# Performance work log

Hardware: AMD Instinct MI355X
Metric: run time of the kernel (lower is better)

Reference implementation:

```python
import jax, jax.numpy as jnp
import numpy as np

C = 1.0           # Poincare ball curvature magnitude (k = -1/c with c=1)
MIN_NORM = 1e-15
PROJ_EPS = 4e-3   # geoopt float32 boundary eps


def _artanh(x):
    return jnp.arctanh(jnp.clip(x, -1.0 + 1e-7, 1.0 - 1e-7))


def _norm(x):
    return jnp.maximum(jnp.linalg.norm(x, axis=-1, keepdims=True), MIN_NORM)


def mobius_matvec(W, x, c=C):
    # geoopt pmath.mobius_matvec with k=-c
    sc = jnp.sqrt(c)
    x_norm = _norm(x)
    Mx = x @ W.T
    Mx_norm = _norm(Mx)
    return jnp.tanh(Mx_norm / x_norm * _artanh(sc * x_norm)) * Mx / (Mx_norm * sc)


def mobius_add(x, y, c=C):
    x2 = jnp.sum(x * x, axis=-1, keepdims=True)
    y2 = jnp.sum(y * y, axis=-1, keepdims=True)
    xy = jnp.sum(x * y, axis=-1, keepdims=True)
    num = (1.0 + 2.0 * c * xy + c * y2) * x + (1.0 - c * x2) * y
    den = 1.0 + 2.0 * c * xy + c * c * x2 * y2
    return num / jnp.maximum(den, MIN_NORM)


def project(x, c=C):
    norm = _norm(x)
    maxnorm = (1.0 - PROJ_EPS) / jnp.sqrt(c)
    return jnp.where(norm > maxnorm, x / norm * maxnorm, x)


def expmap0(u, c=C):
    sc = jnp.sqrt(c)
    un = _norm(u)
    return jnp.tanh(sc * un) * u / (sc * un)


def mobius_linear(x, W, b, c=C):
    # hyperbolic_input=True, hyperbolic_bias=True, nonlin=None
    out = mobius_matvec(W, x, c)
    out = mobius_add(out, b, c)
    return project(out, c)


def setup_inputs() -> dict:
    key = jax.random.key(0)
    ks = jax.random.split(key, 7)
    N, D = 2048, 1024        # batch*tlen, input_size
    V = 32000                # output_size (vocab)
    SLEN, B, CV = 512, 32, 500
    hidden = jax.random.normal(ks[0], (N, D), jnp.float32) * 0.1
    hidden = project(hidden)
    attn = jax.random.uniform(ks[1], (N, SLEN), jnp.float32)
    src_map = jax.random.uniform(ks[2], (SLEN, B, CV), jnp.float32)
    W = jax.random.normal(ks[3], (V, D), jnp.float32) * 0.01
    b = expmap0(jax.random.normal(ks[4], (V,), jnp.float32) / 4.0)
    Wc = jax.random.normal(ks[5], (1, D), jnp.float32) * 0.01
    bc = expmap0(jax.random.normal(ks[6], (1,), jnp.float32) / 4.0)
    return {"hidden": hidden, "attn": attn, "src_map": src_map,
            "W": W, "b": b, "Wc": Wc, "bc": bc, "pad_idx": 1}


def reference(hidden, attn, src_map, W, b, Wc, bc, pad_idx):
    slen, batch, cvocab = src_map.shape
    logits = mobius_linear(hidden, W, b)                  # (N, V)
    logits = logits.at[:, pad_idx].set(-jnp.inf)
    prob = jax.nn.softmax(logits, axis=1)
    p_copy = jax.nn.sigmoid(mobius_linear(hidden, Wc, bc))  # (N, 1)
    out_prob = prob * (1.0 - p_copy)
    mul_attn = attn * p_copy                              # (N, slen)
    a = mul_attn.reshape(-1, batch, slen)                 # (tlen, batch, slen)
    copy_prob = jnp.einsum('tbs,sbc->tbc', a, src_map).reshape(-1, cvocab)
    return jnp.concatenate([out_prob, copy_prob], axis=1)
```

## Files before the change

kernel.cpp:

```cpp
#include <hip/hip_runtime.h>
#include <stdint.h>

#define N_ROWS   2048
#define D_IN     1024
#define V_OUT    32000
#define SLEN_C   512
#define BATCH_C  32
#define CVOC     500
#define OUT_COLS 32500

#define MIN_NORM_F 1e-15f
#define PROJ_EPS_F 4e-3f

typedef __bf16 bf16x8_t __attribute__((ext_vector_type(8)));
typedef float  f32x4_t  __attribute__((ext_vector_type(4)));
typedef unsigned short ushort8_t __attribute__((ext_vector_type(8)));

__device__ __forceinline__ unsigned short f2bf(float f) {
    uint32_t b = __float_as_uint(f);
    b += 0x7FFFu + ((b >> 16) & 1u);
    return (unsigned short)(b >> 16);
}
__device__ __forceinline__ float bf2f(unsigned short u) {
    return __uint_as_float(((uint32_t)u) << 16);
}
__device__ __forceinline__ float wave_sum(float v) {
#pragma unroll
    for (int off = 32; off > 0; off >>= 1) v += __shfl_down(v, off, 64);
    return v;
}

__device__ __forceinline__ void load_lds16(const void* g, void* l) {
    __builtin_amdgcn_global_load_lds(
        (const __attribute__((address_space(1))) void*)g,
        (__attribute__((address_space(3))) void*)l, 16, 0, 0);
}

__global__ __launch_bounds__(256)
void cast_f32_to_bf16(const float* __restrict__ src, unsigned short* __restrict__ dst, int n4) {
    int i = blockIdx.x * blockDim.x + threadIdx.x;
    int stride = gridDim.x * blockDim.x;
    for (; i < n4; i += stride) {
        float4 v = ((const float4*)src)[i];
        ushort4 o;
        o.x = f2bf(v.x); o.y = f2bf(v.y); o.z = f2bf(v.z); o.w = f2bf(v.w);
        ((ushort4*)dst)[i] = o;
    }
}

__global__ __launch_bounds__(256)
void row_stats(const float* __restrict__ hidden, const float* __restrict__ Wc,
               const float* __restrict__ bc_in, float* __restrict__ g_arr,
               float* __restrict__ pc_arr) {
    __shared__ float red[8];
    const int n = blockIdx.x;
    const int tid = threadIdx.x;
    float4 hv = *(const float4*)(hidden + (size_t)n * D_IN + tid * 4);
    float4 wv = *(const float4*)(Wc + tid * 4);
    float s = hv.x * hv.x + hv.y * hv.y + hv.z * hv.z + hv.w * hv.w;
    float d = hv.x * wv.x + hv.y * wv.y + hv.z * wv.z + hv.w * wv.w;
    s = wave_sum(s); d = wave_sum(d);
    const int w = tid >> 6, l = tid & 63;
    if (l == 0) { red[w] = s; red[4 + w] = d; }
    __syncthreads();
    if (tid == 0) {
        float S  = red[0] + red[1] + red[2] + red[3];
        float Dc = red[4] + red[5] + red[6] + red[7];
        float xn = fmaxf(sqrtf(S), MIN_NORM_F);
        float xc = fminf(xn, 1.f - 1e-7f);
        float at = 0.5f * logf((1.f + xc) / (1.f - xc));
        float g = at / xn;
        float mxn = fmaxf(fabsf(Dc), MIN_NORM_F);
        float res = tanhf(mxn * g) * (Dc / mxn);
        float bcv = bc_in[0];
        float x2 = res * res, y2 = bcv * bcv, xyv = res * bcv;
        float num = (1.f + 2.f * xyv + y2) * res + (1.f - x2) * bcv;
        float dn  = fmaxf(1.f + 2.f * xyv + x2 * y2, MIN_NORM_F);
        float o = num / dn;
        float an = fmaxf(fabsf(o), MIN_NORM_F);
        float mxp = 1.f - PROJ_EPS_F;
        if (an > mxp) o = o / an * mxp;
        pc_arr[n] = 1.f / (1.f + expf(-o));
        g_arr[n]  = g;
    }
}


#define STG_A(bufi, chunk, kti) \
    load_lds16(Ag + (size_t)(am0 + ((chunk) << 6) + wave8 + srow) * D_IN + ((kti) << 6) + sk, \
               &Asmem[bufi][(((chunk) << 6) + wave8) << 6])
#define STG_B(bufi, chunk, kti) \
    load_lds16(Bg + (size_t)(bn0 + ((chunk) << 6) + wave8 + srow) * D_IN + ((kti) << 6) + sk, \
               &Bsmem[bufi][(((chunk) << 6) + wave8) << 6])

#define VMCNT(N) \
    __builtin_amdgcn_sched_barrier(0); \
    asm volatile("s_waitcnt vmcnt(" #N ")" ::: "memory"); \
    __builtin_amdgcn_sched_barrier(0);

#define RD_A(RB, MH) \
    _Pragma("unroll") for (int i = 0; i < 4; ++i) { \
        const int r_ = (wm + (MH)*64 + i*16 + fr) << 6; \
        af0[i] = *(const bf16x8_t*)&Asmem[RB][r_ + e0]; \
        af1[i] = *(const bf16x8_t*)&Asmem[RB][r_ + e1]; }

#define RD_B(RB, J0) \
    _Pragma("unroll") for (int j = 0; j < 2; ++j) { \
        const int r_ = (wn + ((J0) + j)*16 + fr) << 6; \
        bf0[(J0)+j] = *(const bf16x8_t*)&Bsmem[RB][r_ + e0]; \
        bf1[(J0)+j] = *(const bf16x8_t*)&Bsmem[RB][r_ + e1]; }

#define MM(MH, J0) \
    __builtin_amdgcn_sched_barrier(0); \
    __builtin_amdgcn_s_barrier(); \
    asm volatile("s_waitcnt lgkmcnt(0)" ::: "memory"); \
    __builtin_amdgcn_sched_barrier(0); \
    __builtin_amdgcn_s_setprio(1); \
    _Pragma("unroll") for (int i = 0; i < 4; ++i) \
        _Pragma("unroll") for (int j = 0; j < 2; ++j) { \
            acc[(MH)*4+i][(J0)+j] = __builtin_amdgcn_mfma_f32_16x16x32_bf16(af0[i], bf0[(J0)+j], acc[(MH)*4+i][(J0)+j], 0, 0, 0); \
            acc[(MH)*4+i][(J0)+j] = __builtin_amdgcn_mfma_f32_16x16x32_bf16(af1[i], bf1[(J0)+j], acc[(MH)*4+i][(J0)+j], 0, 0, 0); } \
    __builtin_amdgcn_s_setprio(0); \
    __builtin_amdgcn_s_barrier(); \
    __builtin_amdgcn_sched_barrier(0);

__global__ __launch_bounds__(512, 2)
void gemm_bt_bf16(const unsigned short* __restrict__ Ag,
                  const unsigned short* __restrict__ Bg,
                  unsigned short* __restrict__ Cb)
{
    __shared__ __align__(16) unsigned short Asmem[2][256 * 64];
    __shared__ __align__(16) unsigned short Bsmem[2][256 * 64];
    const int tid  = threadIdx.x;
    const int wave = tid >> 6;
    const int lane = tid & 63;

    const int f   = blockIdx.x;
    const int swz = (f & 7) * 125 + (f >> 3);
    const int am0 = (swz & 7) * 256;
    const int bn0 = (swz >> 3) * 256;

    const int wr = wave >> 2, wc = wave & 3;
    const int wm = wr * 128, wn = wc * 64;
    const int fr  = lane & 15;
    const int fkb = (lane >> 4) << 4;
    const int swzr = (fr & 7) << 4;
    const int e0 = (fkb ^ swzr) >> 1;
    const int e1 = ((64 + fkb) ^ swzr) >> 1;
    const int wave8 = wave << 3;
    const int srow  = lane >> 3;
    const int sk    = ((lane & 7) ^ srow) << 3;

    f32x4_t acc[8][4] = {};
    bf16x8_t af0[4], af1[4], bf0[4], bf1[4];

    STG_A(0, 0, 0); STG_A(0, 1, 0); STG_A(0, 2, 0); STG_A(0, 3, 0);
    STG_B(0, 0, 0); STG_B(0, 1, 0); STG_B(0, 2, 0); STG_B(0, 3, 0);
    STG_A(1, 0, 1); STG_A(1, 2, 1);
    VMCNT(2)
    __builtin_amdgcn_s_barrier();

    for (int t = 0; t < 7; ++t) {
        const int k1 = 2 * t + 1, k2 = 2 * t + 2, k3 = 2 * t + 3;
        RD_A(0, 0); RD_B(0, 0); STG_B(1, 0, k1); STG_B(1, 1, k1); MM(0, 0);
        RD_B(0, 2);             STG_B(1, 2, k1); STG_B(1, 3, k1); MM(0, 2);
        RD_A(0, 1);             STG_A(1, 1, k1); STG_A(1, 3, k1); MM(1, 0);
        STG_A(0, 0, k2); STG_A(0, 2, k2);
        VMCNT(2)                                                  MM(1, 2);
        RD_A(1, 0); RD_B(1, 0); STG_B(0, 0, k2); STG_B(0, 1, k2); MM(0, 0);
        RD_B(1, 2);             STG_B(0, 2, k2); STG_B(0, 3, k2); MM(0, 2);
        RD_A(1, 1);             STG_A(0, 1, k2); STG_A(0, 3, k2);
                                STG_A(1, 0, k3); STG_A(1, 2, k3); MM(1, 0);
        VMCNT(2)                                                  MM(1, 2);
    }
    RD_A(0, 0); RD_B(0, 0); STG_B(1, 0, 15); STG_B(1, 1, 15); MM(0, 0);
    RD_B(0, 2);             STG_B(1, 2, 15); STG_B(1, 3, 15); MM(0, 2);
    RD_A(0, 1);             STG_A(1, 1, 15); STG_A(1, 3, 15); MM(1, 0);
    VMCNT(0)                                                  MM(1, 2);
    RD_A(1, 0); RD_B(1, 0); MM(0, 0);
    RD_B(1, 2);             MM(0, 2);
    RD_A(1, 1);             MM(1, 0);
                            MM(1, 2);

    const int cm = (lane >> 4) << 2;
    const int cn = lane & 15;
#pragma unroll
    for (int I = 0; I < 8; ++I) {
#pragma unroll
        for (int J = 0; J < 4; ++J) {
            const int mg = am0 + wm + I * 16 + cm;
            const int ng = bn0 + wn + J * 16 + cn;
            unsigned short* cp = Cb + (size_t)mg * (OUT_COLS * 2) + ng;
#pragma unroll
            for (int r = 0; r < 4; ++r)
                cp[(size_t)r * (OUT_COLS * 2)] = f2bf(acc[I][J][r]);
        }
    }
}

__global__ __launch_bounds__(1024)
void softmax_epi(float* __restrict__ Cout, const float* __restrict__ bvec,
                 const float* __restrict__ g_arr, const float* __restrict__ pc_arr,
                 const int* __restrict__ pad_ptr) {
    __shared__ unsigned short mxls[V_OUT];
    __shared__ float red[48];
    __shared__ float bcast[4];
    const int n = blockIdx.x;
    const int tid = threadIdx.x;
    float* row = Cout + (size_t)n * OUT_COLS;
    const unsigned short* rowb = (const unsigned short*)row;
    const int pad = *pad_ptr;

    float s1 = 0.f, s2 = 0.f, s3 = 0.f;
    for (int i = tid * 8; i < V_OUT; i += 8192) {
        ushort8_t mu = *(const ushort8_t*)(rowb + i);
        float4 b0 = *(const float4*)(bvec + i);
        float4 b1 = *(const float4*)(bvec + i + 4);
        float m0 = bf2f(mu[0]), m1 = bf2f(mu[1]), m2 = bf2f(mu[2]), m3 = bf2f(mu[3]);
        float m4 = bf2f(mu[4]), m5 = bf2f(mu[5]), m6 = bf2f(mu[6]), m7 = bf2f(mu[7]);
        s1 += (m0*m0 + m1*m1 + m2*m2 + m3*m3) + (m4*m4 + m5*m5 + m6*m6 + m7*m7);
        s2 += (m0*b0.x + m1*b0.y + m2*b0.z + m3*b0.w) + (m4*b1.x + m5*b1.y + m6*b1.z + m7*b1.w);
        s3 += (b0.x*b0.x + b0.y*b0.y + b0.z*b0.z + b0.w*b0.w)
            + (b1.x*b1.x + b1.y*b1.y + b1.z*b1.z + b1.w*b1.w);
        *(ushort8_t*)&mxls[i] = mu;
    }
    s1 = wave_sum(s1); s2 = wave_sum(s2); s3 = wave_sum(s3);
    const int w = tid >> 6, l = tid & 63;
    if (l == 0) { red[w] = s1; red[16 + w] = s2; red[32 + w] = s3; }
    __syncthreads();
    if (tid == 0) {
        float S1 = 0.f, S2 = 0.f, Sb = 0.f;
        for (int k = 0; k < 16; ++k) { S1 += red[k]; S2 += red[16 + k]; Sb += red[32 + k]; }
        const float g  = g_arr[n];
        const float r   = fmaxf(sqrtf(S1), MIN_NORM_F);
        const float t   = tanhf(r * g);
        const float smv = t / r;
        const float x2 = smv * smv * S1;
        const float xy = smv * S2;
        const float den = fmaxf(1.f + 2.f * xy + x2 * Sb, MIN_NORM_F);
        float P = (1.f + 2.f * xy + Sb) * smv / den;
        float Q = (1.f - x2) / den;
        const float nrm = fmaxf(sqrtf(P * P * S1 + 2.f * P * Q * S2 + Q * Q * Sb), MIN_NORM_F);
        const float mxp = 1.f - PROJ_EPS_F;
        if (nrm > mxp) { const float fsc = mxp / nrm; P *= fsc; Q *= fsc; }
        bcast[0] = P; bcast[1] = Q;
    }
    __syncthreads();
    const float P = bcast[0], Q = bcast[1];

    float z = 0.f;
    for (int i = tid * 8; i < V_OUT; i += 8192) {
        ushort8_t mu = *(const ushort8_t*)&mxls[i];
        float4 b0 = *(const float4*)(bvec + i);
        float4 b1 = *(const float4*)(bvec + i + 4);
        float e0 = __expf(fmaf(P, bf2f(mu[0]), Q * b0.x));
        float e1 = __expf(fmaf(P, bf2f(mu[1]), Q * b0.y));
        float e2 = __expf(fmaf(P, bf2f(mu[2]), Q * b0.z));
        float e3 = __expf(fmaf(P, bf2f(mu[3]), Q * b0.w));
        float e4 = __expf(fmaf(P, bf2f(mu[4]), Q * b1.x));
        float e5 = __expf(fmaf(P, bf2f(mu[5]), Q * b1.y));
        float e6 = __expf(fmaf(P, bf2f(mu[6]), Q * b1.z));
        float e7 = __expf(fmaf(P, bf2f(mu[7]), Q * b1.w));
        if (i + 0 == pad) e0 = 0.f;
        if (i + 1 == pad) e1 = 0.f;
        if (i + 2 == pad) e2 = 0.f;
        if (i + 3 == pad) e3 = 0.f;
        if (i + 4 == pad) e4 = 0.f;
        if (i + 5 == pad) e5 = 0.f;
        if (i + 6 == pad) e6 = 0.f;
        if (i + 7 == pad) e7 = 0.f;
        z += ((e0 + e1) + (e2 + e3)) + ((e4 + e5) + (e6 + e7));
        ushort8_t eu;
        eu[0] = f2bf(e0); eu[1] = f2bf(e1); eu[2] = f2bf(e2); eu[3] = f2bf(e3);
        eu[4] = f2bf(e4); eu[5] = f2bf(e5); eu[6] = f2bf(e6); eu[7] = f2bf(e7);
        *(ushort8_t*)&mxls[i] = eu;
    }
    z = wave_sum(z);
    if (l == 0) red[w] = z;
    __syncthreads();
    if (tid == 0) {
        float a = 0.f;
        for (int k = 0; k < 16; ++k) a += red[k];
        bcast[2] = a;
    }
    __syncthreads();
    const float scale = (1.f - pc_arr[n]) / bcast[2];

    for (int i = tid * 8; i < V_OUT; i += 8192) {
        ushort8_t eu = *(const ushort8_t*)&mxls[i];
        float4 o0, o1;
        o0.x = bf2f(eu[0]) * scale; o0.y = bf2f(eu[1]) * scale;
        o0.z = bf2f(eu[2]) * scale; o0.w = bf2f(eu[3]) * scale;
        o1.x = bf2f(eu[4]) * scale; o1.y = bf2f(eu[5]) * scale;
        o1.z = bf2f(eu[6]) * scale; o1.w = bf2f(eu[7]) * scale;
        *(float4*)(row + i) = o0;
        *(float4*)(row + i + 4) = o1;
    }
}

__global__ __launch_bounds__(128)
void copy_einsum(const float* __restrict__ attn, const float* __restrict__ src_map,
                 const float* __restrict__ pc_arr, float* __restrict__ Cout) {
    __shared__ float atile[32][128];
    const int tid = threadIdx.x;
    const int cc = blockIdx.x;
    const int b  = blockIdx.y;
    const int t0 = blockIdx.z * 32;
    const int c = cc * 128 + tid;
    const bool cv = (c < CVOC);

    float acc[32];
#pragma unroll
    for (int t = 0; t < 32; ++t) acc[t] = 0.f;

    for (int s0 = 0; s0 < SLEN_C; s0 += 128) {
        __syncthreads();
        for (int idx = tid; idx < 32 * 128; idx += 128) {
            const int t = idx >> 7, s = idx & 127;
            atile[t][s] = attn[(size_t)((t0 + t) * BATCH_C + b) * SLEN_C + s0 + s];
        }
        __syncthreads();
        for (int j = 0; j < 128; j += 4) {
            float sv0 = 0.f, sv1 = 0.f, sv2 = 0.f, sv3 = 0.f;
            if (cv) {
                const float* sp = src_map + (size_t)(s0 + j) * (BATCH_C * CVOC) + b * CVOC + c;
                sv0 = sp[0];
                sv1 = sp[BATCH_C * CVOC];
                sv2 = sp[2 * BATCH_C * CVOC];
                sv3 = sp[3 * BATCH_C * CVOC];
            }
#pragma unroll
            for (int t = 0; t < 32; ++t) {
                const float4 av = *(const float4*)&atile[t][j];
                acc[t] = fmaf(av.x, sv0, acc[t]);
                acc[t] = fmaf(av.y, sv1, acc[t]);
                acc[t] = fmaf(av.z, sv2, acc[t]);
                acc[t] = fmaf(av.w, sv3, acc[t]);
            }
        }
    }
    if (cv) {
#pragma unroll
        for (int t = 0; t < 32; ++t) {
            const int n = (t0 + t) * BATCH_C + b;
            Cout[(size_t)n * OUT_COLS + V_OUT + c] = acc[t] * pc_arr[n];
        }
    }
}

extern "C" void kernel_launch(void* const* d_in, const int* in_sizes, int n_in,
                              void* d_out, int out_size, void* d_ws, size_t ws_size,
                              hipStream_t stream) {
    const float* hidden  = (const float*)d_in[0];
    const float* attn    = (const float*)d_in[1];
    const float* src_map = (const float*)d_in[2];
    const float* W       = (const float*)d_in[3];
    const float* bvec    = (const float*)d_in[4];
    const float* Wc      = (const float*)d_in[5];
    const float* bc      = (const float*)d_in[6];
    const int*   padp    = (const int*)d_in[7];
    float* out = (float*)d_out;

    const int wb_elems = V_OUT * D_IN;
    const int hb_elems = N_ROWS * D_IN;
    unsigned short* Wb = (unsigned short*)d_ws;
    unsigned short* Hb = Wb + wb_elems;
    float* g_arr  = (float*)(Hb + hb_elems);
    float* pc_arr = g_arr + N_ROWS;

    cast_f32_to_bf16<<<4000, 256, 0, stream>>>(W, Wb, wb_elems / 4);
    cast_f32_to_bf16<<<512, 256, 0, stream>>>(hidden, Hb, hb_elems / 4);
    row_stats<<<N_ROWS, 256, 0, stream>>>(hidden, Wc, bc, g_arr, pc_arr);

    gemm_bt_bf16<<<1000, 512, 0, stream>>>(Hb, Wb, (unsigned short*)out);

    softmax_epi<<<N_ROWS, 1024, 0, stream>>>(out, bvec, g_arr, pc_arr, padp);

    dim3 egrid(4, BATCH_C, 2);
    copy_einsum<<<egrid, 128, 0, stream>>>(attn, src_map, pc_arr, out);
}
```

Before: 761.0 us.

## Reorder GEMM global-to-LDS staging to prefetch B earlier with deeper vmcnt

Restructures the software-pipelined main loop of the bf16 GEMM so B-tile loads for the next K step are issued a half-iteration earlier, alongside the A halves. The wait threshold rises from 2 to 6 outstanding loads, which keeps more global loads in flight while MFMAs run. The aim is to hide global memory latency better, at the cost of tighter correctness requirements on LDS buffer reuse ordering and possibly more in-flight register or LDS pressure.

```diff
diff --git a/kernel.cpp b/kernel.cpp
--- a/kernel.cpp
+++ b/kernel.cpp
@@ -154,28 +154,29 @@
     f32x4_t acc[8][4] = {};
     bf16x8_t af0[4], af1[4], bf0[4], bf1[4];
 
-    STG_A(0, 0, 0); STG_A(0, 1, 0); STG_A(0, 2, 0); STG_A(0, 3, 0);
-    STG_B(0, 0, 0); STG_B(0, 1, 0); STG_B(0, 2, 0); STG_B(0, 3, 0);
-    STG_A(1, 0, 1); STG_A(1, 2, 1);
-    VMCNT(2)
+    STG_A(0, 0, 0); STG_A(0, 2, 0); STG_B(0, 0, 0); STG_B(0, 1, 0);
+    STG_B(0, 2, 0); STG_B(0, 3, 0); STG_A(0, 1, 0); STG_A(0, 3, 0);
+    STG_A(1, 0, 1); STG_A(1, 2, 1); STG_B(1, 0, 1); STG_B(1, 1, 1);
+    STG_B(1, 2, 1); STG_B(1, 3, 1);
+    VMCNT(6)
     __builtin_amdgcn_s_barrier();
 
     for (int t = 0; t < 7; ++t) {
-        const int k1 = 2 * t + 1, k2 = 2 * t + 2, k3 = 2 * t + 3;
-        RD_A(0, 0); RD_B(0, 0); STG_B(1, 0, k1); STG_B(1, 1, k1); MM(0, 0);
-        RD_B(0, 2);             STG_B(1, 2, k1); STG_B(1, 3, k1); MM(0, 2);
-        RD_A(0, 1);             STG_A(1, 1, k1); STG_A(1, 3, k1); MM(1, 0);
-        STG_A(0, 0, k2); STG_A(0, 2, k2);
-        VMCNT(2)                                                  MM(1, 2);
-        RD_A(1, 0); RD_B(1, 0); STG_B(0, 0, k2); STG_B(0, 1, k2); MM(0, 0);
-        RD_B(1, 2);             STG_B(0, 2, k2); STG_B(0, 3, k2); MM(0, 2);
-        RD_A(1, 1);             STG_A(0, 1, k2); STG_A(0, 3, k2);
-                                STG_A(1, 0, k3); STG_A(1, 2, k3); MM(1, 0);
-        VMCNT(2)                                                  MM(1, 2);
-    }
-    RD_A(0, 0); RD_B(0, 0); STG_B(1, 0, 15); STG_B(1, 1, 15); MM(0, 0);
-    RD_B(0, 2);             STG_B(1, 2, 15); STG_B(1, 3, 15); MM(0, 2);
-    RD_A(0, 1);             STG_A(1, 1, 15); STG_A(1, 3, 15); MM(1, 0);
+        const int T1 = 2 * t + 1, T2 = 2 * t + 2, T3 = 2 * t + 3;
+        RD_A(0, 0); RD_B(0, 0); STG_A(1, 1, T1); STG_A(1, 3, T1); MM(0, 0);
+        RD_B(0, 2);             STG_A(0, 0, T2); STG_A(0, 2, T2); MM(0, 2);
+        RD_A(0, 1);             STG_B(0, 0, T2); STG_B(0, 1, T2); MM(1, 0);
+                                STG_B(0, 2, T2); STG_B(0, 3, T2);
+        VMCNT(6)                                                  MM(1, 2);
+        RD_A(1, 0); RD_B(1, 0); STG_A(0, 1, T2); STG_A(0, 3, T2); MM(0, 0);
+        RD_B(1, 2);             STG_A(1, 0, T3); STG_A(1, 2, T3); MM(0, 2);
+        RD_A(1, 1);             STG_B(1, 0, T3); STG_B(1, 1, T3); MM(1, 0);
+                                STG_B(1, 2, T3); STG_B(1, 3, T3);
+        VMCNT(6)                                                  MM(1, 2);
+    }
+    RD_A(0, 0); RD_B(0, 0); STG_A(1, 1, 15); STG_A(1, 3, 15); MM(0, 0);
+    RD_B(0, 2);                                               MM(0, 2);
+    RD_A(0, 1);                                               MM(1, 0);
     VMCNT(0)                                                  MM(1, 2);
     RD_A(1, 0); RD_B(1, 0); MM(0, 0);
     RD_B(1, 2);             MM(0, 2);
```

Result: faster. 732.6 us (-3.7%).
